# Performance work log

Measured on AMD Instinct MI355X. Metric: run time of the kernel, lower is better.

The kernel has to match this reference:

```python
import jax, jax.numpy as jnp
import numpy as np

B, C, H, W = 8, 256, 128, 128
KC, VC, HEADS = 256, 256, 2
HK, HV = KC // HEADS, VC // HEADS
EPS = 1e-5


def setup_inputs() -> dict:
    key = jax.random.key(0)
    ks = jax.random.split(key, 10)
    s = 0.02  # init scale for weights
    return {
        "x": jax.random.normal(ks[0], (B, C, H, W), jnp.float32),
        "bn_gamma": jnp.ones((C,), jnp.float32),
        "bn_beta": jnp.zeros((C,), jnp.float32),
        "wk": jax.random.normal(ks[1], (KC, C), jnp.float32) * s,
        "bk": jnp.zeros((KC,), jnp.float32),
        "wq": jax.random.normal(ks[2], (KC, C), jnp.float32) * s,
        "bq": jnp.zeros((KC,), jnp.float32),
        "wv": jax.random.normal(ks[3], (VC, C), jnp.float32) * s,
        "bv": jnp.zeros((VC,), jnp.float32),
        "w_fc1": jax.random.normal(ks[4], (HEADS, HEADS), jnp.float32) * 0.5,
        "b_fc1": jnp.zeros((HEADS,), jnp.float32),
        "w_fc2": jax.random.normal(ks[5], (HEADS, HEADS), jnp.float32) * 0.5,
        "b_fc2": jnp.zeros((HEADS,), jnp.float32),
        "w_se": jax.random.normal(ks[6], (HEADS,), jnp.float32) * 0.5,  # Conv2d(heads,1,1) weight
        "b_se": jnp.zeros((), jnp.float32),
        "w_rep": jax.random.normal(ks[7], (C, C), jnp.float32) * s,
        "b_rep": jnp.zeros((C,), jnp.float32),
    }


def reference(x, bn_gamma, bn_beta, wk, bk, wq, bq, wv, bv,
              w_fc1, b_fc1, w_fc2, b_fc2, w_se, b_se, w_rep, b_rep):
    n, c, h, w = x.shape
    s = h * w
    # BatchNorm2d (training-mode math: batch statistics over N,H,W)
    mean = x.mean(axis=(0, 2, 3))
    var = x.var(axis=(0, 2, 3))
    xn = (x - mean[None, :, None, None]) * jax.lax.rsqrt(var + EPS)[None, :, None, None]
    xn = xn * bn_gamma[None, :, None, None] + bn_beta[None, :, None, None]
    xr = xn.reshape(n, c, s)  # [B, C, HW]
    # 1x1 convs == per-pixel channel matmuls
    k = jnp.einsum('oc,bcs->bos', wk, xr) + bk[None, :, None]
    q = jnp.einsum('oc,bcs->bos', wq, xr) + bq[None, :, None]
    v = jnp.einsum('oc,bcs->bos', wv, xr) + bv[None, :, None]
    # split heads: [B, HEADS, hk, S]
    k = jax.nn.softmax(k.reshape(n, HEADS, HK, s), axis=-1)   # softmax over spatial
    q = jax.nn.softmax(q.reshape(n, HEADS, HK, s), axis=2)    # softmax over channel
    v = v.reshape(n, HEADS, HV, s)
    # linear-attention context: key @ value^T -> [B, HEADS, hk, hv]
    context = jnp.einsum('bnks,bnvs->bnkv', k, v)
    # SE block over head channel (in_channels = HEADS, reduction = 1)
    pooled = context.mean(axis=(2, 3))                              # [B, HEADS]
    gate = jax.nn.sigmoid(jax.nn.relu(pooled @ w_fc1.T + b_fc1) @ w_fc2.T + b_fc2)
    gated = context * gate[:, :, None, None]
    ctx = jnp.einsum('n,bnkv->bkv', w_se, gated) + b_se             # Conv2d(HEADS,1,1): [B, hk, hv]
    # second pass: ctx^T @ query per head, concat over heads -> [B, C, S]
    out = jnp.einsum('bkv,bnks->bnvs', ctx, q).reshape(n, c, s)
    out = jnp.einsum('oc,bcs->bos', w_rep, out) + b_rep[None, :, None]
    return out.reshape(n, c, h, w)
```

## Files before the change

### kernel.cpp

```cpp
#include <hip/hip_runtime.h>
#include <hip/hip_bf16.h>

#define BATCH 8
#define CH 256
#define SPAT 16384
#define TP 64
#define PITCH 272

typedef __attribute__((ext_vector_type(4))) float f32x4;
typedef __attribute__((ext_vector_type(8))) __bf16 bf16x8;
typedef __attribute__((ext_vector_type(4))) __bf16 bf16x4;

#define WS_ROWSUM  512
#define WS_POOLED  2560
#define WS_BKF     2576
#define WS_BQF     2832
#define WS_BVF     3088
#define WS_SUM     3344
#define WS_SSUM    3600
#define WS_CTX     4096
#define WS_MBF     266240
#define WS_WKBF    528384
#define WS_WQBF    561152
#define WS_WVBF    593920

__device__ __forceinline__ int lswz(int h) { return h ^ (((h >> 7) & 7) << 3); }

__device__ __forceinline__ void blockReduce2(float& a, float& b, volatile float* sm) {
    int lane = threadIdx.x & 63, w = threadIdx.x >> 6;
#pragma unroll
    for (int o = 32; o; o >>= 1) { a += __shfl_down(a, o); b += __shfl_down(b, o); }
    if (lane == 0) { sm[w] = a; sm[4 + w] = b; }
    __syncthreads();
    if (threadIdx.x == 0) {
        a = sm[0] + sm[1] + sm[2] + sm[3];
        b = sm[4] + sm[5] + sm[6] + sm[7];
    }
}

__global__ __launch_bounds__(256) void ea_bnstats(const float* __restrict__ x,
                                                  float* sums, float* ssums) {
    __shared__ float sm[8];
    int bi = blockIdx.x, c = bi >> 3, b = bi & 7;
    const float4* p = (const float4*)(x + (size_t)(b * CH + c) * SPAT);
    float sum = 0.f, ss = 0.f;
    for (int i = threadIdx.x; i < SPAT / 4; i += 256) {
        float4 v = p[i];
        sum += v.x + v.y + v.z + v.w;
        ss  += v.x * v.x + v.y * v.y + v.z * v.z + v.w * v.w;
    }
    blockReduce2(sum, ss, sm);
    if (threadIdx.x == 0) { atomicAdd(sums + c, sum); atomicAdd(ssums + c, ss); }
}

__global__ __launch_bounds__(256) void ea_fold(const float* __restrict__ wk, const float* __restrict__ wq,
        const float* __restrict__ wv, const float* __restrict__ bk, const float* __restrict__ bq,
        const float* __restrict__ bv, const float* __restrict__ gamma, const float* __restrict__ beta,
        const float* __restrict__ sums, const float* __restrict__ ssums,
        __bf16* wkb, __bf16* wqb, __bf16* wvb, float* bkf, float* bqf, float* bvf) {
    __shared__ float sm[12];
    int o = blockIdx.x, c = threadIdx.x;
    const float inv = 1.f / (float)(BATCH * SPAT);
    float mean = sums[c] * inv;
    float var  = ssums[c] * inv - mean * mean;
    float sc   = gamma[c] * rsqrtf(var + 1e-5f);
    float sh   = beta[c] - mean * sc;
    float k = wk[o * 256 + c], q = wq[o * 256 + c], v = wv[o * 256 + c];
    wkb[o * 256 + c] = (__bf16)(k * sc);
    wqb[o * 256 + c] = (__bf16)(q * sc);
    wvb[o * 256 + c] = (__bf16)(v * sc);
    float ak = k * sh, aq = q * sh, av = v * sh;
    int lane = c & 63, w = c >> 6;
#pragma unroll
    for (int off = 32; off; off >>= 1) {
        ak += __shfl_down(ak, off);
        aq += __shfl_down(aq, off);
        av += __shfl_down(av, off);
    }
    if (lane == 0) { sm[w] = ak; sm[4 + w] = aq; sm[8 + w] = av; }
    __syncthreads();
    if (c == 0) {
        bkf[o] = bk[o] + sm[0] + sm[1] + sm[2] + sm[3];
        bqf[o] = bq[o] + sm[4] + sm[5] + sm[6] + sm[7];
        bvf[o] = bv[o] + sm[8] + sm[9] + sm[10] + sm[11];
    }
}

__global__ __launch_bounds__(512, 2) void ea_kvctx(const float* __restrict__ x,
        const __bf16* __restrict__ wkb, const __bf16* __restrict__ wvb,
        const float* __restrict__ bkf, const float* __restrict__ bvf,
        float* __restrict__ ctxpart, float* __restrict__ rowsum) {
    __shared__ __bf16 Xl[2 * 64 * 256];
    __shared__ __bf16 Pl[256 * 64];
    __shared__ __bf16 Vl[256 * 64];
    const int bi = blockIdx.x, b = bi >> 5, chunk = bi & 31;
    const int t = threadIdx.x;
    const int lane = t & 63, wave = t >> 6, quad = lane >> 4, l15 = lane & 15;
    const int rbase = wave * 32;
    const int sl = t & 15, cg = t >> 4;
    const int xswz = (sl & 7) << 3;
    const float* xp0 = x + (size_t)(b * CH + cg * 8) * SPAT + chunk * 512 + 4 * sl;

    float bkr[2][4], bvr[2][4];
#pragma unroll
    for (int mt = 0; mt < 2; mt++)
#pragma unroll
        for (int r = 0; r < 4; r++) {
            int row = rbase + mt * 16 + quad * 4 + r;
            bkr[mt][r] = bkf[row];
            bvr[mt][r] = bvf[row];
        }

    const f32x4 z = {0.f, 0.f, 0.f, 0.f};
    f32x4 cacc[4][4];
#pragma unroll
    for (int vt = 0; vt < 4; vt++)
#pragma unroll
        for (int kt = 0; kt < 4; kt++) cacc[vt][kt] = z;
    float rs_acc[2][4] = {{0.f, 0.f, 0.f, 0.f}, {0.f, 0.f, 0.f, 0.f}};

    const int head = wave >> 2, rh = (wave >> 1) & 1, chh = wave & 1;
    const int prow0 = head * 128 + rh * 64, vrow0 = head * 128 + chh * 64;

    f32x4 xr[8];
#pragma unroll
    for (int i = 0; i < 8; i++) xr[i] = *(const f32x4*)(xp0 + (size_t)i * SPAT);
#pragma unroll
    for (int i = 0; i < 8; i++) {
        int ca = (cg * 8 + i) ^ xswz;
#pragma unroll
        for (int j = 0; j < 4; j++)
            Xl[(4 * sl + j) * 256 + ca] = (__bf16)xr[i][j];
    }
    __syncthreads();

    int buf = 0;
    for (int tt = 0; tt < 8; tt++) {
        const __bf16* Xb = Xl + buf * (64 * 256);
        f32x4 ak[2][4], av[2][4];
#pragma unroll
        for (int mt = 0; mt < 2; mt++)
#pragma unroll
            for (int nt = 0; nt < 4; nt++) { ak[mt][nt] = z; av[mt][nt] = z; }
#pragma unroll 2
        for (int ks = 0; ks < 8; ks++) {
            int k0 = ks * 32 + quad * 8;
            bf16x8 bb[4];
#pragma unroll
            for (int nt = 0; nt < 4; nt++)
                bb[nt] = *(const bf16x8*)(Xb + (4 * l15 + nt) * 256 + (k0 ^ ((l15 & 7) << 3)));
            bf16x8 aK[2], aV[2];
#pragma unroll
            for (int mt = 0; mt < 2; mt++) {
                size_t off = (size_t)(rbase + mt * 16 + l15) * 256 + k0;
                aK[mt] = *(const bf16x8*)(wkb + off);
                aV[mt] = *(const bf16x8*)(wvb + off);
            }
#pragma unroll
            for (int mt = 0; mt < 2; mt++)
#pragma unroll
                for (int nt = 0; nt < 4; nt++) {
                    ak[mt][nt] = __builtin_amdgcn_mfma_f32_16x16x32_bf16(aK[mt], bb[nt], ak[mt][nt], 0, 0, 0);
                    av[mt][nt] = __builtin_amdgcn_mfma_f32_16x16x32_bf16(aV[mt], bb[nt], av[mt][nt], 0, 0, 0);
                }
        }
        if (tt < 7) {
            const float* xp = xp0 + (tt + 1) * 64;
#pragma unroll
            for (int i = 0; i < 8; i++) xr[i] = *(const f32x4*)(xp + (size_t)i * SPAT);
        }
#pragma unroll
        for (int mt = 0; mt < 2; mt++)
#pragma unroll
            for (int r = 0; r < 4; r++) {
                int row = rbase + mt * 16 + quad * 4 + r;
                float bK = bkr[mt][r], bV = bvr[mt][r];
                float e0 = __expf(ak[mt][0][r] + bK);
                float e1 = __expf(ak[mt][1][r] + bK);
                float e2 = __expf(ak[mt][2][r] + bK);
                float e3 = __expf(ak[mt][3][r] + bK);
                rs_acc[mt][r] += e0 + e1 + e2 + e3;
                int pa = row * 64 + ((4 * l15) ^ ((row & 7) << 3));
                bf16x4 pk = {(__bf16)e0, (__bf16)e1, (__bf16)e2, (__bf16)e3};
                *(bf16x4*)(Pl + pa) = pk;
                bf16x4 vk = {(__bf16)(av[mt][0][r] + bV), (__bf16)(av[mt][1][r] + bV),
                             (__bf16)(av[mt][2][r] + bV), (__bf16)(av[mt][3][r] + bV)};
                *(bf16x4*)(Vl + pa) = vk;
            }
        __syncthreads();
#pragma unroll
        for (int ks = 0; ks < 2; ks++) {
            int k0 = ks * 32 + quad * 8;
            bf16x8 pfr[4], vfr[4];
#pragma unroll
            for (int kt = 0; kt < 4; kt++) {
                int row = prow0 + kt * 16 + l15;
                pfr[kt] = *(const bf16x8*)(Pl + row * 64 + (k0 ^ ((row & 7) << 3)));
            }
#pragma unroll
            for (int vt = 0; vt < 4; vt++) {
                int row = vrow0 + vt * 16 + l15;
                vfr[vt] = *(const bf16x8*)(Vl + row * 64 + (k0 ^ ((row & 7) << 3)));
            }
#pragma unroll
            for (int vt = 0; vt < 4; vt++)
#pragma unroll
                for (int kt = 0; kt < 4; kt++)
                    cacc[vt][kt] = __builtin_amdgcn_mfma_f32_16x16x32_bf16(vfr[vt], pfr[kt], cacc[vt][kt], 0, 0, 0);
        }
        if (tt < 7) {
            __bf16* Xn = Xl + (buf ^ 1) * (64 * 256);
#pragma unroll
            for (int i = 0; i < 8; i++) {
                int ca = (cg * 8 + i) ^ xswz;
#pragma unroll
                for (int j = 0; j < 4; j++)
                    Xn[(4 * sl + j) * 256 + ca] = (__bf16)xr[i][j];
            }
        }
        __syncthreads();
        buf ^= 1;
    }
#pragma unroll
    for (int mt = 0; mt < 2; mt++)
#pragma unroll
        for (int r = 0; r < 4; r++) {
            float v = rs_acc[mt][r];
            v += __shfl_xor(v, 1);
            v += __shfl_xor(v, 2);
            v += __shfl_xor(v, 4);
            v += __shfl_xor(v, 8);
            if (l15 == 0)
                atomicAdd(rowsum + b * CH + rbase + mt * 16 + quad * 4 + r, v);
        }
    float* pbase = ctxpart + (((size_t)(b * 32 + chunk)) * 2 + head) * 16384;
#pragma unroll
    for (int vt = 0; vt < 4; vt++)
#pragma unroll
        for (int kt = 0; kt < 4; kt++) {
            int kk = rh * 64 + kt * 16 + l15;
            int vv = chh * 64 + vt * 16 + quad * 4;
            *(f32x4*)(pbase + kk * 128 + vv) = cacc[vt][kt];
        }
}

__global__ __launch_bounds__(256) void ea_ctxred(const float* __restrict__ part,
        const float* __restrict__ rowsum, float* __restrict__ ctx, float* __restrict__ pooled) {
    __shared__ float sm[8];
    int bi = blockIdx.x, b = bi >> 5, h = (bi >> 4) & 1, ks = bi & 15;
    int t = threadIdx.x;
    int kk = ks * 8 + (t >> 5), vv = (t & 31) * 4;
    const float* p0 = part + (((size_t)b * 32) * 2 + h) * 16384 + (size_t)kk * 128 + vv;
    f32x4 acc = {0.f, 0.f, 0.f, 0.f};
#pragma unroll 4
    for (int c = 0; c < 32; c++) {
        f32x4 v = *(const f32x4*)(p0 + (size_t)c * 32768);
        acc[0] += v[0]; acc[1] += v[1]; acc[2] += v[2]; acc[3] += v[3];
    }
    float inv = 1.f / rowsum[b * CH + h * 128 + kk];
    f32x4 o = {acc[0] * inv, acc[1] * inv, acc[2] * inv, acc[3] * inv};
    *(f32x4*)(ctx + ((size_t)b * 2 + h) * 16384 + (size_t)kk * 128 + vv) = o;
    float s = o[0] + o[1] + o[2] + o[3], d = 0.f;
    blockReduce2(s, d, sm);
    if (t == 0) atomicAdd(pooled + b * 2 + h, s);
}

__global__ __launch_bounds__(256) void ea_M(const float* ctx, const float* pooled,
                                            const float* wfc1, const float* bfc1,
                                            const float* wfc2, const float* bfc2,
                                            const float* wse, const float* bse,
                                            const float* wrep, __bf16* Mbf) {
    __shared__ float L[128 * 128];
    int bi = blockIdx.x, b = bi >> 3, h = (bi >> 2) & 1, strip = bi & 3;
    float p0 = pooled[b * 2] * (1.f / 16384.f), p1 = pooled[b * 2 + 1] * (1.f / 16384.f);
    float z10 = fmaxf(0.f, wfc1[0] * p0 + wfc1[1] * p1 + bfc1[0]);
    float z11 = fmaxf(0.f, wfc1[2] * p0 + wfc1[3] * p1 + bfc1[1]);
    float z20 = wfc2[0] * z10 + wfc2[1] * z11 + bfc2[0];
    float z21 = wfc2[2] * z10 + wfc2[3] * z11 + bfc2[1];
    float g0 = 1.f / (1.f + __expf(-z20)), g1 = 1.f / (1.f + __expf(-z21));
    float a0 = wse[0] * g0, a1 = wse[1] * g1, bs = bse[0];
    const float* c0 = ctx + (size_t)b * 2 * 16384;
    const float* c1 = c0 + 16384;
    for (int i = threadIdx.x; i < 16384; i += 256) L[i] = a0 * c0[i] + a1 * c1[i] + bs;
    __syncthreads();
    int o = strip * 64 + (threadIdx.x & 63), kb = (threadIdx.x >> 6) * 32;
    const float4* wr = (const float4*)(wrep + (size_t)o * 256 + h * 128);
    for (int kk = kb; kk < kb + 32; kk++) {
        const float4* Lr = (const float4*)(L + kk * 128);
        float acc = 0.f;
#pragma unroll 8
        for (int j = 0; j < 32; j++) {
            float4 w4 = wr[j];
            float4 l4 = Lr[j];
            acc += w4.x * l4.x + w4.y * l4.y + w4.z * l4.z + w4.w * l4.w;
        }
        Mbf[(size_t)(b * 256 + o) * 256 + h * 128 + kk] = (__bf16)acc;
    }
}

__device__ __forceinline__ void stage_x(const float* xb, __bf16* Xl, int t) {
    int l15 = t & 15, c0 = t >> 4;
    const float* xp = xb + l15 * 4;
    int hbase = (l15 * 4) * PITCH;
#pragma unroll
    for (int i = 0; i < 16; i++) {
        int c = c0 * 16 + i;
        float4 v = *(const float4*)(xp + (size_t)c * SPAT);
        Xl[lswz(hbase + c)]             = (__bf16)v.x;
        Xl[lswz(hbase + PITCH + c)]     = (__bf16)v.y;
        Xl[lswz(hbase + 2 * PITCH + c)] = (__bf16)v.z;
        Xl[lswz(hbase + 3 * PITCH + c)] = (__bf16)v.w;
    }
}

__device__ __forceinline__ void mm256(const __bf16* __restrict__ A, const __bf16* Xl,
                                      int WB, int quad, int l15, f32x4 (&acc)[4][4]) {
#pragma unroll 2
    for (int ks = 0; ks < 8; ks++) {
        int k0 = ks * 32;
        bf16x8 a[4];
#pragma unroll
        for (int mt = 0; mt < 4; mt++)
            a[mt] = *(const bf16x8*)(A + (WB + mt * 16 + l15) * 256 + k0 + quad * 8);
        bf16x8 bb[4];
#pragma unroll
        for (int nt = 0; nt < 4; nt++)
            bb[nt] = *(const bf16x8*)(Xl + lswz((4 * l15 + nt) * PITCH + k0 + quad * 8));
#pragma unroll
        for (int mt = 0; mt < 4; mt++)
#pragma unroll
            for (int nt = 0; nt < 4; nt++)
                acc[mt][nt] = __builtin_amdgcn_mfma_f32_16x16x32_bf16(a[mt], bb[nt], acc[mt][nt], 0, 0, 0);
    }
}

__global__ __launch_bounds__(256) void ea_final(const float* __restrict__ x,
        const __bf16* __restrict__ wqb, const float* __restrict__ bqf,
        const __bf16* __restrict__ Mbf, const float* __restrict__ brep, float* __restrict__ out) {
    __shared__ __bf16 X[TP * PITCH];
    __shared__ __bf16 Q[TP * PITCH];
    __shared__ float psum[256];
    __shared__ float rcp[TP * 2];
    int bi = blockIdx.x, b = bi >> 8, s0 = (bi & 255) * TP, t = threadIdx.x;
    stage_x(x + (size_t)b * CH * SPAT + s0, X, t);
    __syncthreads();

    int lane = t & 63, wave = t >> 6, quad = lane >> 4, l15 = lane & 15, WB = wave * 64;
    const f32x4 z = {0.f, 0.f, 0.f, 0.f};

    {
        f32x4 acc[4][4];
#pragma unroll
        for (int mt = 0; mt < 4; mt++)
#pragma unroll
            for (int nt = 0; nt < 4; nt++) acc[mt][nt] = z;
        mm256(wqb, X, WB, quad, l15, acc);
#pragma unroll
        for (int mt = 0; mt < 4; mt++) {
            int row0 = WB + mt * 16 + quad * 4;
#pragma unroll
            for (int nt = 0; nt < 4; nt++) {
                bf16x4 qk;
#pragma unroll
                for (int r = 0; r < 4; r++)
                    qk[r] = (__bf16)__expf(acc[mt][nt][r] + bqf[row0 + r]);
                *(bf16x4*)(Q + lswz((4 * l15 + nt) * PITCH + row0)) = qk;
            }
        }
    }
    __syncthreads();
    {
        int px = t & 63, hh = (t >> 6) & 1, part = t >> 7;
        int cb = hh * 128 + part * 64;
        float s = 0.f;
#pragma unroll
        for (int j = 0; j < 8; j++) {
            bf16x8 qv = *(const bf16x8*)(Q + lswz(px * PITCH + cb + j * 8));
#pragma unroll
            for (int e = 0; e < 8; e++) s += (float)qv[e];
        }
        psum[t] = s;
    }
    __syncthreads();
    if (t < 128) {
        float tot = psum[t] + psum[t + 128];
        rcp[(t & 63) * 2 + (t >> 6)] = 1.f / tot;
    }
    __syncthreads();
#pragma unroll 2
    for (int e = t; e < TP * 32; e += 256) {
        int px = e >> 5, cc = (e & 31) * 8;
        float sc = rcp[px * 2 + (cc >> 7)];
        int h = lswz(px * PITCH + cc);
        bf16x8 qv = *(const bf16x8*)(Q + h);
        bf16x8 qo;
#pragma unroll
        for (int j2 = 0; j2 < 8; j2++) qo[j2] = (__bf16)((float)qv[j2] * sc);
        *(bf16x8*)(Q + h) = qo;
    }
    __syncthreads();
    {
        f32x4 acc[4][4];
#pragma unroll
        for (int mt = 0; mt < 4; mt++)
#pragma unroll
            for (int nt = 0; nt < 4; nt++) acc[mt][nt] = z;
        mm256(Mbf + (size_t)b * 65536, Q, WB, quad, l15, acc);
#pragma unroll
        for (int mt = 0; mt < 4; mt++) {
            int row0 = WB + mt * 16 + quad * 4;
#pragma unroll
            for (int r = 0; r < 4; r++) {
                int row = row0 + r;
                float bs = brep[row];
                f32x4 o4 = {acc[mt][0][r] + bs, acc[mt][1][r] + bs,
                            acc[mt][2][r] + bs, acc[mt][3][r] + bs};
                *(f32x4*)(out + (size_t)(b * CH + row) * SPAT + s0 + 4 * l15) = o4;
            }
        }
    }
}

extern "C" void kernel_launch(void* const* d_in, const int* in_sizes, int n_in,
                              void* d_out, int out_size, void* d_ws, size_t ws_size,
                              hipStream_t stream) {
    (void)in_sizes; (void)n_in; (void)out_size; (void)ws_size;
    const float* x     = (const float*)d_in[0];
    const float* gamma = (const float*)d_in[1];
    const float* beta  = (const float*)d_in[2];
    const float* wk    = (const float*)d_in[3];
    const float* bk    = (const float*)d_in[4];
    const float* wq    = (const float*)d_in[5];
    const float* bq    = (const float*)d_in[6];
    const float* wv    = (const float*)d_in[7];
    const float* bv    = (const float*)d_in[8];
    const float* wfc1  = (const float*)d_in[9];
    const float* bfc1  = (const float*)d_in[10];
    const float* wfc2  = (const float*)d_in[11];
    const float* bfc2  = (const float*)d_in[12];
    const float* wse   = (const float*)d_in[13];
    const float* bse   = (const float*)d_in[14];
    const float* wrep  = (const float*)d_in[15];
    const float* brep  = (const float*)d_in[16];

    float* ws = (float*)d_ws;
    __bf16* wkb = (__bf16*)(ws + WS_WKBF);
    __bf16* wqb = (__bf16*)(ws + WS_WQBF);
    __bf16* wvb = (__bf16*)(ws + WS_WVBF);
    __bf16* Mbf = (__bf16*)(ws + WS_MBF);

    float* ctxpart = (float*)d_out;
    float* out = (float*)d_out;

    hipMemsetAsync((void*)(ws + WS_ROWSUM), 0,
                   (size_t)(WS_CTX - WS_ROWSUM) * sizeof(float), stream);
    ea_bnstats<<<2048, 256, 0, stream>>>(x, ws + WS_SUM, ws + WS_SSUM);
    ea_fold<<<256, 256, 0, stream>>>(wk, wq, wv, bk, bq, bv, gamma, beta,
                                     ws + WS_SUM, ws + WS_SSUM,
                                     wkb, wqb, wvb, ws + WS_BKF, ws + WS_BQF, ws + WS_BVF);
    ea_kvctx<<<256, 512, 0, stream>>>(x, wkb, wvb, ws + WS_BKF, ws + WS_BVF,
                                      ctxpart, ws + WS_ROWSUM);
    ea_ctxred<<<256, 256, 0, stream>>>(ctxpart, ws + WS_ROWSUM, ws + WS_CTX, ws + WS_POOLED);
    ea_M<<<64, 256, 0, stream>>>(ws + WS_CTX, ws + WS_POOLED, wfc1, bfc1, wfc2, bfc2,
                                 wse, bse, wrep, Mbf);
    ea_final<<<2048, 256, 0, stream>>>(x, wqb, ws + WS_BQF, Mbf, brep, out);
}
```

Before: 593.7 us.

## Alias X and Q LDS tiles, vectorize bf16 staging stores, raise ea_final occupancy

The final kernel now uses a single 64x256 bf16 LDS buffer for both the staged input and the softmaxed query, with an XOR swizzle instead of padded pitch. An extra barrier makes it safe to overwrite X with Q after the first matmul. Staging stores are packed into 16-byte bf16x8 writes instead of scalar writes, in both ea_final and the context kernel. Launch bounds request 3 blocks per CU, and the bn-stats loop is unrolled. Halving LDS per block aims for more concurrent blocks, at the cost of register pressure and one more barrier.

```diff
diff --git a/kernel.cpp b/kernel.cpp
--- a/kernel.cpp
+++ b/kernel.cpp
@@ -5,7 +5,6 @@
 #define CH 256
 #define SPAT 16384
 #define TP 64
-#define PITCH 272
 
 typedef __attribute__((ext_vector_type(4))) float f32x4;
 typedef __attribute__((ext_vector_type(8))) __bf16 bf16x8;
@@ -24,8 +23,6 @@
 #define WS_WQBF    561152
 #define WS_WVBF    593920
 
-__device__ __forceinline__ int lswz(int h) { return h ^ (((h >> 7) & 7) << 3); }
-
 __device__ __forceinline__ void blockReduce2(float& a, float& b, volatile float* sm) {
     int lane = threadIdx.x & 63, w = threadIdx.x >> 6;
 #pragma unroll
@@ -44,6 +41,7 @@
     int bi = blockIdx.x, c = bi >> 3, b = bi & 7;
     const float4* p = (const float4*)(x + (size_t)(b * CH + c) * SPAT);
     float sum = 0.f, ss = 0.f;
+#pragma unroll 4
     for (int i = threadIdx.x; i < SPAT / 4; i += 256) {
         float4 v = p[i];
         sum += v.x + v.y + v.z + v.w;
@@ -126,11 +124,11 @@
 #pragma unroll
     for (int i = 0; i < 8; i++) xr[i] = *(const f32x4*)(xp0 + (size_t)i * SPAT);
 #pragma unroll
-    for (int i = 0; i < 8; i++) {
-        int ca = (cg * 8 + i) ^ xswz;
-#pragma unroll
-        for (int j = 0; j < 4; j++)
-            Xl[(4 * sl + j) * 256 + ca] = (__bf16)xr[i][j];
+    for (int j = 0; j < 4; j++) {
+        bf16x8 w;
+#pragma unroll
+        for (int i = 0; i < 8; i++) w[i] = (__bf16)xr[i][j];
+        *(bf16x8*)(Xl + (4 * sl + j) * 256 + ((cg * 8) ^ xswz)) = w;
     }
     __syncthreads();
 
@@ -211,11 +209,11 @@
         if (tt < 7) {
             __bf16* Xn = Xl + (buf ^ 1) * (64 * 256);
 #pragma unroll
-            for (int i = 0; i < 8; i++) {
-                int ca = (cg * 8 + i) ^ xswz;
-#pragma unroll
-                for (int j = 0; j < 4; j++)
-                    Xn[(4 * sl + j) * 256 + ca] = (__bf16)xr[i][j];
+            for (int j = 0; j < 4; j++) {
+                bf16x8 w;
+#pragma unroll
+                for (int i = 0; i < 8; i++) w[i] = (__bf16)xr[i][j];
+                *(bf16x8*)(Xn + (4 * sl + j) * 256 + ((cg * 8) ^ xswz)) = w;
             }
         }
         __syncthreads();
@@ -298,34 +296,19 @@
     }
 }
 
-__device__ __forceinline__ void stage_x(const float* xb, __bf16* Xl, int t) {
-    int l15 = t & 15, c0 = t >> 4;
-    const float* xp = xb + l15 * 4;
-    int hbase = (l15 * 4) * PITCH;
-#pragma unroll
-    for (int i = 0; i < 16; i++) {
-        int c = c0 * 16 + i;
-        float4 v = *(const float4*)(xp + (size_t)c * SPAT);
-        Xl[lswz(hbase + c)]             = (__bf16)v.x;
-        Xl[lswz(hbase + PITCH + c)]     = (__bf16)v.y;
-        Xl[lswz(hbase + 2 * PITCH + c)] = (__bf16)v.z;
-        Xl[lswz(hbase + 3 * PITCH + c)] = (__bf16)v.w;
-    }
-}
-
 __device__ __forceinline__ void mm256(const __bf16* __restrict__ A, const __bf16* Xl,
                                       int WB, int quad, int l15, f32x4 (&acc)[4][4]) {
 #pragma unroll 2
     for (int ks = 0; ks < 8; ks++) {
-        int k0 = ks * 32;
+        int k0 = ks * 32 + quad * 8;
         bf16x8 a[4];
 #pragma unroll
         for (int mt = 0; mt < 4; mt++)
-            a[mt] = *(const bf16x8*)(A + (WB + mt * 16 + l15) * 256 + k0 + quad * 8);
+            a[mt] = *(const bf16x8*)(A + (WB + mt * 16 + l15) * 256 + k0);
         bf16x8 bb[4];
 #pragma unroll
         for (int nt = 0; nt < 4; nt++)
-            bb[nt] = *(const bf16x8*)(Xl + lswz((4 * l15 + nt) * PITCH + k0 + quad * 8));
+            bb[nt] = *(const bf16x8*)(Xl + (4 * l15 + nt) * 256 + (k0 ^ ((l15 & 7) << 3)));
 #pragma unroll
         for (int mt = 0; mt < 4; mt++)
 #pragma unroll
@@ -334,48 +317,68 @@
     }
 }
 
-__global__ __launch_bounds__(256) void ea_final(const float* __restrict__ x,
+__global__ __launch_bounds__(256, 3) void ea_final(const float* __restrict__ x,
         const __bf16* __restrict__ wqb, const float* __restrict__ bqf,
         const __bf16* __restrict__ Mbf, const float* __restrict__ brep, float* __restrict__ out) {
-    __shared__ __bf16 X[TP * PITCH];
-    __shared__ __bf16 Q[TP * PITCH];
+    __shared__ __bf16 XQ[TP * 256];
     __shared__ float psum[256];
     __shared__ float rcp[TP * 2];
     int bi = blockIdx.x, b = bi >> 8, s0 = (bi & 255) * TP, t = threadIdx.x;
-    stage_x(x + (size_t)b * CH * SPAT + s0, X, t);
+
+    {
+        int sl = t & 15, cg = t >> 4;
+        int xswz = (sl & 7) << 3;
+        const float* xp = x + (size_t)(b * CH + cg * 16) * SPAT + s0 + 4 * sl;
+#pragma unroll
+        for (int half = 0; half < 2; half++) {
+            f32x4 xr[8];
+#pragma unroll
+            for (int i = 0; i < 8; i++)
+                xr[i] = *(const f32x4*)(xp + (size_t)(half * 8 + i) * SPAT);
+#pragma unroll
+            for (int j = 0; j < 4; j++) {
+                bf16x8 w;
+#pragma unroll
+                for (int i = 0; i < 8; i++) w[i] = (__bf16)xr[i][j];
+                *(bf16x8*)(XQ + (4 * sl + j) * 256 + ((cg * 16 + half * 8) ^ xswz)) = w;
+            }
+        }
+    }
     __syncthreads();
 
     int lane = t & 63, wave = t >> 6, quad = lane >> 4, l15 = lane & 15, WB = wave * 64;
     const f32x4 z = {0.f, 0.f, 0.f, 0.f};
 
-    {
-        f32x4 acc[4][4];
-#pragma unroll
-        for (int mt = 0; mt < 4; mt++)
-#pragma unroll
-            for (int nt = 0; nt < 4; nt++) acc[mt][nt] = z;
-        mm256(wqb, X, WB, quad, l15, acc);
-#pragma unroll
-        for (int mt = 0; mt < 4; mt++) {
-            int row0 = WB + mt * 16 + quad * 4;
-#pragma unroll
-            for (int nt = 0; nt < 4; nt++) {
-                bf16x4 qk;
-#pragma unroll
-                for (int r = 0; r < 4; r++)
-                    qk[r] = (__bf16)__expf(acc[mt][nt][r] + bqf[row0 + r]);
-                *(bf16x4*)(Q + lswz((4 * l15 + nt) * PITCH + row0)) = qk;
-            }
+    f32x4 acc[4][4];
+#pragma unroll
+    for (int mt = 0; mt < 4; mt++)
+#pragma unroll
+        for (int nt = 0; nt < 4; nt++) acc[mt][nt] = z;
+    mm256(wqb, XQ, WB, quad, l15, acc);
+    __syncthreads();
+
+#pragma unroll
+    for (int mt = 0; mt < 4; mt++) {
+        int row0 = WB + mt * 16 + quad * 4;
+#pragma unroll
+        for (int nt = 0; nt < 4; nt++) {
+            int px = 4 * l15 + nt;
+            bf16x4 qk;
+#pragma unroll
+            for (int r = 0; r < 4; r++)
+                qk[r] = (__bf16)__expf(acc[mt][nt][r] + bqf[row0 + r]);
+            *(bf16x4*)(XQ + px * 256 + (row0 ^ ((l15 & 7) << 3))) = qk;
         }
     }
     __syncthreads();
     {
         int px = t & 63, hh = (t >> 6) & 1, part = t >> 7;
         int cb = hh * 128 + part * 64;
+        int swz = ((px >> 2) & 7) << 3;
         float s = 0.f;
 #pragma unroll
         for (int j = 0; j < 8; j++) {
-            bf16x8 qv = *(const bf16x8*)(Q + lswz(px * PITCH + cb + j * 8));
+            bf16x8 qv = *(const bf16x8*)(XQ + px * 256 + ((cb + j * 8) ^ swz));
 #pragma unroll
             for (int e = 0; e < 8; e++) s += (float)qv[e];
         }
@@ -391,32 +394,29 @@
     for (int e = t; e < TP * 32; e += 256) {
         int px = e >> 5, cc = (e & 31) * 8;
         float sc = rcp[px * 2 + (cc >> 7)];
-        int h = lswz(px * PITCH + cc);
-        bf16x8 qv = *(const bf16x8*)(Q + h);
+        int h = px * 256 + (cc ^ (((px >> 2) & 7) << 3));
+        bf16x8 qv = *(const bf16x8*)(XQ + h);
         bf16x8 qo;
 #pragma unroll
         for (int j2 = 0; j2 < 8; j2++) qo[j2] = (__bf16)((float)qv[j2] * sc);
-        *(bf16x8*)(Q + h) = qo;
-    }
-    __syncthreads();
-    {
-        f32x4 acc[4][4];
-#pragma unroll
-        for (int mt = 0; mt < 4; mt++)
-#pragma unroll
-            for (int nt = 0; nt < 4; nt++) acc[mt][nt] = z;
-        mm256(Mbf + (size_t)b * 65536, Q, WB, quad, l15, acc);
-#pragma unroll
-        for (int mt = 0; mt < 4; mt++) {
-            int row0 = WB + mt * 16 + quad * 4;
-#pragma unroll
-            for (int r = 0; r < 4; r++) {
-                int row = row0 + r;
-                float bs = brep[row];
-                f32x4 o4 = {acc[mt][0][r] + bs, acc[mt][1][r] + bs,
-                            acc[mt][2][r] + bs, acc[mt][3][r] + bs};
-                *(f32x4*)(out + (size_t)(b * CH + row) * SPAT + s0 + 4 * l15) = o4;
-            }
+        *(bf16x8*)(XQ + h) = qo;
+    }
+    __syncthreads();
+#pragma unroll
+    for (int mt = 0; mt < 4; mt++)
+#pragma unroll
+        for (int nt = 0; nt < 4; nt++) acc[mt][nt] = z;
+    mm256(Mbf + (size_t)b * 65536, XQ, WB, quad, l15, acc);
+#pragma unroll
+    for (int mt = 0; mt < 4; mt++) {
+        int row0 = WB + mt * 16 + quad * 4;
+#pragma unroll
+        for (int r = 0; r < 4; r++) {
+            int row = row0 + r;
+            float bs = brep[row];
+            f32x4 o4 = {acc[mt][0][r] + bs, acc[mt][1][r] + bs,
+                        acc[mt][2][r] + bs, acc[mt][3][r] + bs};
+            *(f32x4*)(out + (size_t)(b * CH + row) * SPAT + s0 + 4 * l15) = o4;
         }
     }
 }
```

New measurement: 575.8 us. 3.0% less time.
